# Performance work log

Measured on AMD Instinct MI355X. Metric: run time of the kernel, lower is better.

The kernel has to match this reference:

```python
import jax, jax.numpy as jnp
import numpy as np

HIDDEN = 2048
NUM_EXPERTS = 64
TOP_K = 2
LOAD_BALANCE_ALPHA = 0.01
Z_LOSS_ALPHA = 1e-4
TEMPERATURE = 1.0  # buffer init, clamped to [0.1, 2.0] -> 1.0


def setup_inputs() -> dict:
    key = jax.random.key(0)
    k1, k2 = jax.random.split(key)
    x = jax.random.normal(k1, (4, 4096, HIDDEN), dtype=jnp.float32)
    W = jax.random.normal(k2, (NUM_EXPERTS, HIDDEN), dtype=jnp.float32) * (1.0 / np.sqrt(HIDDEN))
    return {"x": x, "W": W}


def reference(x, W):
    # Eval-mode forward of RuchbahMoEGate.
    B, S, H = x.shape
    x_flat = x.reshape(-1, H)                       # [N, H], N = B*S
    logits = jnp.einsum('nh,eh->ne', x_flat, W)     # gate projection, [N, E]
    logits = logits / TEMPERATURE                   # temp clamped to [0.1,2.0]
    scores = jax.nn.softmax(logits, axis=-1)        # [N, E]
    # top-k routing (eval: dynamic top-k == top_k, no capacity limitation)
    top_scores, top_idx = jax.lax.top_k(scores, TOP_K)   # [N, K]
    top_scores = jax.nn.softmax(top_scores.astype(jnp.float32), axis=-1).astype(x.dtype)
    # load-balance loss (eval: total_routing_count == 0 -> basic term only)
    expert_load = scores.mean(axis=0)               # [E]
    ideal_load = 1.0 / NUM_EXPERTS
    lb_loss = LOAD_BALANCE_ALPHA * jnp.sum((expert_load - ideal_load) ** 2)
    # z-loss: penalize large logit logsumexp
    z_loss = Z_LOSS_ALPHA * jnp.mean(jax.nn.logsumexp(logits, axis=-1) ** 2)
    total_loss = lb_loss + z_loss
    return top_scores, top_idx, total_loss
```

## Files before the change

### kernel.cpp

```cpp
#include <hip/hip_runtime.h>
#include <cstdint>
#include <cstddef>

#define HDIM 2048
#define NEXP 64
#define HC   16
#define BTOK 128
#define GTHR 128
#define PX   132
#define PW   68
#define GATE_TOK 16

__global__ __launch_bounds__(GTHR) void moe_gemm(const float* __restrict__ x,
                                                 const float* __restrict__ W,
                                                 float* __restrict__ partial,
                                                 int N, int HS) {
  __shared__ __align__(16) float xt[2][HC][PX];
  __shared__ __align__(16) float wt[2][HC][PW];

  const int ntb   = N / BTOK;
  const int tb    = blockIdx.x % ntb;
  const int hsIdx = blockIdx.x / ntb;
  const int tok0  = tb * BTOK;
  const int h0    = hsIdx * HS;
  const int tid   = threadIdx.x;
  const int lane  = tid & 63;
  const int wid   = tid >> 6;
  const int xoff  = wid * 64 + (lane >> 3) * 8;
  const int e0    = (lane & 7) * 8;
  const int srow  = tid >> 2;
  const int sj    = (tid & 3) * 4;

  float acc[8][8];
#pragma unroll
  for (int t = 0; t < 8; ++t)
#pragma unroll
    for (int e = 0; e < 8; ++e) acc[t][e] = 0.f;

  float4 xr[4], wr[2];

#pragma unroll
  for (int i = 0; i < 4; ++i)
    xr[i] = *reinterpret_cast<const float4*>(&x[(size_t)(tok0 + srow + i * 32) * HDIM + h0 + sj]);
#pragma unroll
  for (int i = 0; i < 2; ++i)
    wr[i] = *reinterpret_cast<const float4*>(&W[(size_t)(srow + i * 32) * HDIM + h0 + sj]);
#pragma unroll
  for (int i = 0; i < 4; ++i) {
    const int r = srow + i * 32;
    xt[0][sj + 0][r] = xr[i].x; xt[0][sj + 1][r] = xr[i].y;
    xt[0][sj + 2][r] = xr[i].z; xt[0][sj + 3][r] = xr[i].w;
  }
#pragma unroll
  for (int i = 0; i < 2; ++i) {
    const int r = srow + i * 32;
    wt[0][sj + 0][r] = wr[i].x; wt[0][sj + 1][r] = wr[i].y;
    wt[0][sj + 2][r] = wr[i].z; wt[0][sj + 3][r] = wr[i].w;
  }
  __syncthreads();

  const int niter = HS / HC;
  int cur = 0;
  for (int c = 0; c < niter; ++c) {
    if (c + 1 < niter) {
      const int hb = h0 + (c + 1) * HC;
#pragma unroll
      for (int i = 0; i < 4; ++i)
        xr[i] = *reinterpret_cast<const float4*>(&x[(size_t)(tok0 + srow + i * 32) * HDIM + hb + sj]);
#pragma unroll
      for (int i = 0; i < 2; ++i)
        wr[i] = *reinterpret_cast<const float4*>(&W[(size_t)(srow + i * 32) * HDIM + hb + sj]);
    }
#pragma unroll
    for (int h = 0; h < HC; ++h) {
      const float4 a0 = *reinterpret_cast<const float4*>(&xt[cur][h][xoff]);
      const float4 a1 = *reinterpret_cast<const float4*>(&xt[cur][h][xoff + 4]);
      const float4 b0 = *reinterpret_cast<const float4*>(&wt[cur][h][e0]);
      const float4 b1 = *reinterpret_cast<const float4*>(&wt[cur][h][e0 + 4]);
      const float xs[8] = {a0.x, a0.y, a0.z, a0.w, a1.x, a1.y, a1.z, a1.w};
      const float wv[8] = {b0.x, b0.y, b0.z, b0.w, b1.x, b1.y, b1.z, b1.w};
#pragma unroll
      for (int t = 0; t < 8; ++t)
#pragma unroll
        for (int e = 0; e < 8; ++e)
          acc[t][e] = fmaf(xs[t], wv[e], acc[t][e]);
    }
    if (c + 1 < niter) {
      const int nx = cur ^ 1;
#pragma unroll
      for (int i = 0; i < 4; ++i) {
        const int r = srow + i * 32;
        xt[nx][sj + 0][r] = xr[i].x; xt[nx][sj + 1][r] = xr[i].y;
        xt[nx][sj + 2][r] = xr[i].z; xt[nx][sj + 3][r] = xr[i].w;
      }
#pragma unroll
      for (int i = 0; i < 2; ++i) {
        const int r = srow + i * 32;
        wt[nx][sj + 0][r] = wr[i].x; wt[nx][sj + 1][r] = wr[i].y;
        wt[nx][sj + 2][r] = wr[i].z; wt[nx][sj + 3][r] = wr[i].w;
      }
    }
    __syncthreads();
    cur ^= 1;
  }

  const size_t base = ((size_t)hsIdx * N + (tok0 + xoff)) * NEXP + e0;
#pragma unroll
  for (int t = 0; t < 8; ++t) {
    *reinterpret_cast<float4*>(&partial[base + (size_t)t * NEXP]) =
        make_float4(acc[t][0], acc[t][1], acc[t][2], acc[t][3]);
    *reinterpret_cast<float4*>(&partial[base + (size_t)t * NEXP + 4]) =
        make_float4(acc[t][4], acc[t][5], acc[t][6], acc[t][7]);
  }
}

template <int HSPLIT>
__global__ __launch_bounds__(256) void moe_gate(const float* __restrict__ partial,
                                                int N,
                                                float* __restrict__ outS,
                                                float* __restrict__ outI,
                                                float* __restrict__ esumP,
                                                float* __restrict__ lse2P) {
  __shared__ float es[4][NEXP];
  __shared__ float l2[4];
  const int tid  = threadIdx.x;
  const int lane = tid & 63;
  const int w    = tid >> 6;
  const int base = blockIdx.x * GATE_TOK + w * 4;

  float esum = 0.f, lse2 = 0.f;
#pragma unroll
  for (int tt = 0; tt < 4; ++tt) {
    const int t = base + tt;
    float logit = 0.f;
#pragma unroll
    for (int hs = 0; hs < HSPLIT; ++hs)
      logit += partial[((size_t)hs * N + t) * NEXP + lane];

    float m = logit;
#pragma unroll
    for (int d = 1; d < 64; d <<= 1) m = fmaxf(m, __shfl_xor(m, d));
    const float p = expf(logit - m);
    float s = p;
#pragma unroll
    for (int d = 1; d < 64; d <<= 1) s += __shfl_xor(s, d);
    const float score = p / s;

    float v1 = score; int i1 = lane;
#pragma unroll
    for (int d = 1; d < 64; d <<= 1) {
      const float pv = __shfl_xor(v1, d);
      const int   pi = __shfl_xor(i1, d);
      if (pv > v1 || (pv == v1 && pi < i1)) { v1 = pv; i1 = pi; }
    }
    float v2 = (lane == i1) ? -1.f : score; int i2 = lane;
#pragma unroll
    for (int d = 1; d < 64; d <<= 1) {
      const float pv = __shfl_xor(v2, d);
      const int   pi = __shfl_xor(i2, d);
      if (pv > v2 || (pv == v2 && pi < i2)) { v2 = pv; i2 = pi; }
    }

    if (lane == 0) {
      const float mx  = fmaxf(v1, v2);
      const float e1  = expf(v1 - mx), e2 = expf(v2 - mx);
      const float inv = 1.f / (e1 + e2);
      *reinterpret_cast<float2*>(&outS[2 * (size_t)t]) = make_float2(e1 * inv, e2 * inv);
      *reinterpret_cast<float2*>(&outI[2 * (size_t)t]) = make_float2((float)i1, (float)i2);
    }

    esum += score;
    const float lse = m + logf(s);
    lse2 += lse * lse;
  }

  es[w][lane] = esum;
  if (lane == 0) l2[w] = lse2;
  __syncthreads();
  if (tid < NEXP)
    esumP[(size_t)blockIdx.x * NEXP + tid] = es[0][tid] + es[1][tid] + es[2][tid] + es[3][tid];
  if (tid == 0)
    lse2P[blockIdx.x] = l2[0] + l2[1] + l2[2] + l2[3];
}

__global__ __launch_bounds__(256) void moe_loss(const float* __restrict__ esumP,
                                                const float* __restrict__ lse2P,
                                                float* __restrict__ outL,
                                                int N, int nb) {
  __shared__ float es[4][NEXP];
  __shared__ float l2s[4];
  const int tid = threadIdx.x, lane = tid & 63, w = tid >> 6;

  float acc = 0.f;
  for (int b = w; b < nb; b += 4) acc += esumP[(size_t)b * NEXP + lane];
  es[w][lane] = acc;

  float la = 0.f;
  for (int b = tid; b < nb; b += 256) la += lse2P[b];
#pragma unroll
  for (int d = 1; d < 64; d <<= 1) la += __shfl_xor(la, d);
  if (lane == 0) l2s[w] = la;
  __syncthreads();

  if (tid < NEXP) {
    const float tot  = es[0][tid] + es[1][tid] + es[2][tid] + es[3][tid];
    const float load = tot / (float)N;
    const float dv   = load - 1.0f / 64.0f;
    float q = dv * dv;
#pragma unroll
    for (int d = 1; d < 64; d <<= 1) q += __shfl_xor(q, d);
    if (tid == 0) {
      const float lseSum = l2s[0] + l2s[1] + l2s[2] + l2s[3];
      outL[0] = 0.01f * q + 1e-4f * (lseSum / (float)N);
    }
  }
}

extern "C" void kernel_launch(void* const* d_in, const int* in_sizes, int n_in,
                              void* d_out, int out_size, void* d_ws, size_t ws_size,
                              hipStream_t stream) {
  const float* x = (const float*)d_in[0];
  const float* W = (const float*)d_in[1];
  const int N  = in_sizes[0] / HDIM;
  const int GB = N / GATE_TOK;

  float* out  = (float*)d_out;
  float* outS = out;
  float* outI = out + (size_t)2 * N;
  float* outL = out + (size_t)4 * N;

  int hsplit = 1;
  for (int h = 8; h >= 1; h >>= 1) {
    const size_t need = (size_t)h * N * NEXP * sizeof(float)
                      + (size_t)GB * (NEXP + 1) * sizeof(float) + 256;
    if (ws_size >= need) { hsplit = h; break; }
  }
  const int HS = HDIM / hsplit;

  float* partial = (float*)d_ws;
  float* esumP   = (float*)((char*)d_ws + (size_t)hsplit * N * NEXP * sizeof(float));
  float* lse2P   = esumP + (size_t)GB * NEXP;

  const int ntb = N / BTOK;
  moe_gemm<<<dim3(ntb * hsplit), dim3(GTHR), 0, stream>>>(x, W, partial, N, HS);
  switch (hsplit) {
    case 8: moe_gate<8><<<dim3(GB), dim3(256), 0, stream>>>(partial, N, outS, outI, esumP, lse2P); break;
    case 4: moe_gate<4><<<dim3(GB), dim3(256), 0, stream>>>(partial, N, outS, outI, esumP, lse2P); break;
    case 2: moe_gate<2><<<dim3(GB), dim3(256), 0, stream>>>(partial, N, outS, outI, esumP, lse2P); break;
    default: moe_gate<1><<<dim3(GB), dim3(256), 0, stream>>>(partial, N, outS, outI, esumP, lse2P); break;
  }
  moe_loss<<<dim3(1), dim3(256), 0, stream>>>(esumP, lse2P, outL, N, GB);
}
```

Measured before the change: 300.7 us.

## Shrink GEMM token tile, batch gate reductions, fuse loss via last-block atomic

The GEMM block shrinks to one 64-thread wavefront covering 64 tokens, which doubles the grid and so raises parallelism across CUs, at the cost of less reuse of W per block. The gate kernel now loads all split partials up front and interleaves the shuffle reductions for four tokens to expose ILP. The separate loss kernel is removed: the last gate block, found with an atomic counter, does the final reduction over a transposed esum buffer. This saves one launch but adds a memset and a fence/atomic per block.

```diff
diff --git a/kernel.cpp b/kernel.cpp
--- a/kernel.cpp
+++ b/kernel.cpp
@@ -5,16 +5,15 @@
 #define HDIM 2048
 #define NEXP 64
 #define HC   16
-#define BTOK 128
-#define GTHR 128
-#define PX   132
+#define BTOK 64
+#define PX   68
 #define PW   68
 #define GATE_TOK 16
 
-__global__ __launch_bounds__(GTHR) void moe_gemm(const float* __restrict__ x,
-                                                 const float* __restrict__ W,
-                                                 float* __restrict__ partial,
-                                                 int N, int HS) {
+__global__ __launch_bounds__(64) void moe_gemm(const float* __restrict__ x,
+                                               const float* __restrict__ W,
+                                               float* __restrict__ partial,
+                                               int N, int HS) {
   __shared__ __align__(16) float xt[2][HC][PX];
   __shared__ __align__(16) float wt[2][HC][PW];
 
@@ -24,10 +23,8 @@
   const int tok0  = tb * BTOK;
   const int h0    = hsIdx * HS;
   const int tid   = threadIdx.x;
-  const int lane  = tid & 63;
-  const int wid   = tid >> 6;
-  const int xoff  = wid * 64 + (lane >> 3) * 8;
-  const int e0    = (lane & 7) * 8;
+  const int xoff  = (tid >> 3) * 8;
+  const int e0    = (tid & 7) * 8;
   const int srow  = tid >> 2;
   const int sj    = (tid & 3) * 4;
 
@@ -37,23 +34,18 @@
 #pragma unroll
     for (int e = 0; e < 8; ++e) acc[t][e] = 0.f;
 
-  float4 xr[4], wr[2];
-
-#pragma unroll
-  for (int i = 0; i < 4; ++i)
-    xr[i] = *reinterpret_cast<const float4*>(&x[(size_t)(tok0 + srow + i * 32) * HDIM + h0 + sj]);
-#pragma unroll
-  for (int i = 0; i < 2; ++i)
-    wr[i] = *reinterpret_cast<const float4*>(&W[(size_t)(srow + i * 32) * HDIM + h0 + sj]);
+  float4 xr[4], wr[4];
+
 #pragma unroll
   for (int i = 0; i < 4; ++i) {
-    const int r = srow + i * 32;
+    xr[i] = *reinterpret_cast<const float4*>(&x[(size_t)(tok0 + srow + i * 16) * HDIM + h0 + sj]);
+    wr[i] = *reinterpret_cast<const float4*>(&W[(size_t)(srow + i * 16) * HDIM + h0 + sj]);
+  }
+#pragma unroll
+  for (int i = 0; i < 4; ++i) {
+    const int r = srow + i * 16;
     xt[0][sj + 0][r] = xr[i].x; xt[0][sj + 1][r] = xr[i].y;
     xt[0][sj + 2][r] = xr[i].z; xt[0][sj + 3][r] = xr[i].w;
-  }
-#pragma unroll
-  for (int i = 0; i < 2; ++i) {
-    const int r = srow + i * 32;
     wt[0][sj + 0][r] = wr[i].x; wt[0][sj + 1][r] = wr[i].y;
     wt[0][sj + 2][r] = wr[i].z; wt[0][sj + 3][r] = wr[i].w;
   }
@@ -65,11 +57,10 @@
     if (c + 1 < niter) {
       const int hb = h0 + (c + 1) * HC;
 #pragma unroll
-      for (int i = 0; i < 4; ++i)
-        xr[i] = *reinterpret_cast<const float4*>(&x[(size_t)(tok0 + srow + i * 32) * HDIM + hb + sj]);
-#pragma unroll
-      for (int i = 0; i < 2; ++i)
-        wr[i] = *reinterpret_cast<const float4*>(&W[(size_t)(srow + i * 32) * HDIM + hb + sj]);
+      for (int i = 0; i < 4; ++i) {
+        xr[i] = *reinterpret_cast<const float4*>(&x[(size_t)(tok0 + srow + i * 16) * HDIM + hb + sj]);
+        wr[i] = *reinterpret_cast<const float4*>(&W[(size_t)(srow + i * 16) * HDIM + hb + sj]);
+      }
     }
 #pragma unroll
     for (int h = 0; h < HC; ++h) {
@@ -89,13 +80,9 @@
       const int nx = cur ^ 1;
 #pragma unroll
       for (int i = 0; i < 4; ++i) {
-        const int r = srow + i * 32;
+        const int r = srow + i * 16;
         xt[nx][sj + 0][r] = xr[i].x; xt[nx][sj + 1][r] = xr[i].y;
         xt[nx][sj + 2][r] = xr[i].z; xt[nx][sj + 3][r] = xr[i].w;
-      }
-#pragma unroll
-      for (int i = 0; i < 2; ++i) {
-        const int r = srow + i * 32;
         wt[nx][sj + 0][r] = wr[i].x; wt[nx][sj + 1][r] = wr[i].y;
         wt[nx][sj + 2][r] = wr[i].z; wt[nx][sj + 3][r] = wr[i].w;
       }
@@ -116,102 +103,142 @@
 
 template <int HSPLIT>
 __global__ __launch_bounds__(256) void moe_gate(const float* __restrict__ partial,
-                                                int N,
+                                                int N, int GB,
                                                 float* __restrict__ outS,
                                                 float* __restrict__ outI,
                                                 float* __restrict__ esumP,
-                                                float* __restrict__ lse2P) {
+                                                float* __restrict__ lse2P,
+                                                unsigned* __restrict__ counter,
+                                                float* __restrict__ outL) {
   __shared__ float es[4][NEXP];
   __shared__ float l2[4];
+  __shared__ float esF[NEXP];
+  __shared__ float l2F[4];
+  __shared__ int lastFlag;
   const int tid  = threadIdx.x;
   const int lane = tid & 63;
   const int w    = tid >> 6;
   const int base = blockIdx.x * GATE_TOK + w * 4;
 
-  float esum = 0.f, lse2 = 0.f;
+  float v[4][HSPLIT];
+#pragma unroll
+  for (int tt = 0; tt < 4; ++tt)
+#pragma unroll
+    for (int hs = 0; hs < HSPLIT; ++hs)
+      v[tt][hs] = partial[((size_t)hs * N + base + tt) * NEXP + lane];
+
+  float logit[4];
 #pragma unroll
   for (int tt = 0; tt < 4; ++tt) {
-    const int t = base + tt;
-    float logit = 0.f;
-#pragma unroll
-    for (int hs = 0; hs < HSPLIT; ++hs)
-      logit += partial[((size_t)hs * N + t) * NEXP + lane];
-
-    float m = logit;
-#pragma unroll
-    for (int d = 1; d < 64; d <<= 1) m = fmaxf(m, __shfl_xor(m, d));
-    const float p = expf(logit - m);
-    float s = p;
-#pragma unroll
-    for (int d = 1; d < 64; d <<= 1) s += __shfl_xor(s, d);
-    const float score = p / s;
-
-    float v1 = score; int i1 = lane;
-#pragma unroll
-    for (int d = 1; d < 64; d <<= 1) {
-      const float pv = __shfl_xor(v1, d);
-      const int   pi = __shfl_xor(i1, d);
-      if (pv > v1 || (pv == v1 && pi < i1)) { v1 = pv; i1 = pi; }
-    }
-    float v2 = (lane == i1) ? -1.f : score; int i2 = lane;
-#pragma unroll
-    for (int d = 1; d < 64; d <<= 1) {
-      const float pv = __shfl_xor(v2, d);
-      const int   pi = __shfl_xor(i2, d);
-      if (pv > v2 || (pv == v2 && pi < i2)) { v2 = pv; i2 = pi; }
-    }
-
-    if (lane == 0) {
-      const float mx  = fmaxf(v1, v2);
-      const float e1  = expf(v1 - mx), e2 = expf(v2 - mx);
+    float s = v[tt][0];
+#pragma unroll
+    for (int hs = 1; hs < HSPLIT; ++hs) s += v[tt][hs];
+    logit[tt] = s;
+  }
+
+  float m[4], p[4], s[4], sc[4];
+#pragma unroll
+  for (int tt = 0; tt < 4; ++tt) m[tt] = logit[tt];
+#pragma unroll
+  for (int d = 1; d < 64; d <<= 1)
+#pragma unroll
+    for (int tt = 0; tt < 4; ++tt) m[tt] = fmaxf(m[tt], __shfl_xor(m[tt], d));
+#pragma unroll
+  for (int tt = 0; tt < 4; ++tt) { p[tt] = expf(logit[tt] - m[tt]); s[tt] = p[tt]; }
+#pragma unroll
+  for (int d = 1; d < 64; d <<= 1)
+#pragma unroll
+    for (int tt = 0; tt < 4; ++tt) s[tt] += __shfl_xor(s[tt], d);
+#pragma unroll
+  for (int tt = 0; tt < 4; ++tt) sc[tt] = p[tt] / s[tt];
+
+  float v1[4]; int i1[4];
+#pragma unroll
+  for (int tt = 0; tt < 4; ++tt) { v1[tt] = sc[tt]; i1[tt] = lane; }
+#pragma unroll
+  for (int d = 1; d < 64; d <<= 1)
+#pragma unroll
+    for (int tt = 0; tt < 4; ++tt) {
+      const float pv = __shfl_xor(v1[tt], d);
+      const int   pi = __shfl_xor(i1[tt], d);
+      if (pv > v1[tt] || (pv == v1[tt] && pi < i1[tt])) { v1[tt] = pv; i1[tt] = pi; }
+    }
+  float v2[4]; int i2[4];
+#pragma unroll
+  for (int tt = 0; tt < 4; ++tt) { v2[tt] = (lane == i1[tt]) ? -1.f : sc[tt]; i2[tt] = lane; }
+#pragma unroll
+  for (int d = 1; d < 64; d <<= 1)
+#pragma unroll
+    for (int tt = 0; tt < 4; ++tt) {
+      const float pv = __shfl_xor(v2[tt], d);
+      const int   pi = __shfl_xor(i2[tt], d);
+      if (pv > v2[tt] || (pv == v2[tt] && pi < i2[tt])) { v2[tt] = pv; i2[tt] = pi; }
+    }
+
+  if (lane == 0) {
+#pragma unroll
+    for (int tt = 0; tt < 4; ++tt) {
+      const int t = base + tt;
+      const float mx  = fmaxf(v1[tt], v2[tt]);
+      const float e1  = expf(v1[tt] - mx), e2 = expf(v2[tt] - mx);
       const float inv = 1.f / (e1 + e2);
       *reinterpret_cast<float2*>(&outS[2 * (size_t)t]) = make_float2(e1 * inv, e2 * inv);
-      *reinterpret_cast<float2*>(&outI[2 * (size_t)t]) = make_float2((float)i1, (float)i2);
-    }
-
-    esum += score;
-    const float lse = m + logf(s);
+      *reinterpret_cast<float2*>(&outI[2 * (size_t)t]) = make_float2((float)i1[tt], (float)i2[tt]);
+    }
+  }
+
+  const float esum = ((sc[0] + sc[1]) + sc[2]) + sc[3];
+  float lse2 = 0.f;
+#pragma unroll
+  for (int tt = 0; tt < 4; ++tt) {
+    const float lse = m[tt] + logf(s[tt]);
     lse2 += lse * lse;
   }
-
   es[w][lane] = esum;
   if (lane == 0) l2[w] = lse2;
   __syncthreads();
   if (tid < NEXP)
-    esumP[(size_t)blockIdx.x * NEXP + tid] = es[0][tid] + es[1][tid] + es[2][tid] + es[3][tid];
+    esumP[(size_t)tid * GB + blockIdx.x] = es[0][tid] + es[1][tid] + es[2][tid] + es[3][tid];
   if (tid == 0)
     lse2P[blockIdx.x] = l2[0] + l2[1] + l2[2] + l2[3];
-}
-
-__global__ __launch_bounds__(256) void moe_loss(const float* __restrict__ esumP,
-                                                const float* __restrict__ lse2P,
-                                                float* __restrict__ outL,
-                                                int N, int nb) {
-  __shared__ float es[4][NEXP];
-  __shared__ float l2s[4];
-  const int tid = threadIdx.x, lane = tid & 63, w = tid >> 6;
-
-  float acc = 0.f;
-  for (int b = w; b < nb; b += 4) acc += esumP[(size_t)b * NEXP + lane];
-  es[w][lane] = acc;
+
+  __threadfence();
+  if (tid == 0) lastFlag = (atomicAdd(counter, 1u) == (unsigned)(GB - 1));
+  __syncthreads();
+  if (!lastFlag) return;
+  __threadfence();
+
+  const int e = tid >> 2, q = tid & 3;
+  const int seg = GB / 4;
+  const float4* colp = reinterpret_cast<const float4*>(&esumP[(size_t)e * GB + q * seg]);
+  float a = 0.f;
+  for (int i = 0; i < seg / 4; ++i) {
+    const float4 t4 = colp[i];
+    a += ((t4.x + t4.y) + t4.z) + t4.w;
+  }
+  a += __shfl_xor(a, 1);
+  a += __shfl_xor(a, 2);
+  if (q == 0) esF[e] = a;
 
   float la = 0.f;
-  for (int b = tid; b < nb; b += 256) la += lse2P[b];
+  for (int i = tid; i * 4 < GB; i += 256) {
+    const float4 t4 = reinterpret_cast<const float4*>(lse2P)[i];
+    la += ((t4.x + t4.y) + t4.z) + t4.w;
+  }
 #pragma unroll
   for (int d = 1; d < 64; d <<= 1) la += __shfl_xor(la, d);
-  if (lane == 0) l2s[w] = la;
+  if (lane == 0) l2F[w] = la;
   __syncthreads();
 
   if (tid < NEXP) {
-    const float tot  = es[0][tid] + es[1][tid] + es[2][tid] + es[3][tid];
-    const float load = tot / (float)N;
+    const float load = esF[tid] / (float)N;
     const float dv   = load - 1.0f / 64.0f;
-    float q = dv * dv;
-#pragma unroll
-    for (int d = 1; d < 64; d <<= 1) q += __shfl_xor(q, d);
+    float qq = dv * dv;
+#pragma unroll
+    for (int d = 1; d < 64; d <<= 1) qq += __shfl_xor(qq, d);
     if (tid == 0) {
-      const float lseSum = l2s[0] + l2s[1] + l2s[2] + l2s[3];
-      outL[0] = 0.01f * q + 1e-4f * (lseSum / (float)N);
+      const float lseSum = ((l2F[0] + l2F[1]) + l2F[2]) + l2F[3];
+      outL[0] = 0.01f * qq + 1e-4f * (lseSum / (float)N);
     }
   }
 }
@@ -232,22 +259,25 @@
   int hsplit = 1;
   for (int h = 8; h >= 1; h >>= 1) {
     const size_t need = (size_t)h * N * NEXP * sizeof(float)
-                      + (size_t)GB * (NEXP + 1) * sizeof(float) + 256;
+                      + (size_t)NEXP * GB * sizeof(float)
+                      + (size_t)GB * sizeof(float) + 256;
     if (ws_size >= need) { hsplit = h; break; }
   }
   const int HS = HDIM / hsplit;
 
-  float* partial = (float*)d_ws;
-  float* esumP   = (float*)((char*)d_ws + (size_t)hsplit * N * NEXP * sizeof(float));
-  float* lse2P   = esumP + (size_t)GB * NEXP;
+  float*    partial = (float*)d_ws;
+  float*    esumP   = (float*)((char*)d_ws + (size_t)hsplit * N * NEXP * 4);
+  float*    lse2P   = esumP + (size_t)NEXP * GB;
+  unsigned* counter = (unsigned*)(lse2P + GB);
+
+  hipMemsetAsync(counter, 0, sizeof(unsigned), stream);
 
   const int ntb = N / BTOK;
-  moe_gemm<<<dim3(ntb * hsplit), dim3(GTHR), 0, stream>>>(x, W, partial, N, HS);
+  moe_gemm<<<dim3(ntb * hsplit), dim3(64), 0, stream>>>(x, W, partial, N, HS);
   switch (hsplit) {
-    case 8: moe_gate<8><<<dim3(GB), dim3(256), 0, stream>>>(partial, N, outS, outI, esumP, lse2P); break;
-    case 4: moe_gate<4><<<dim3(GB), dim3(256), 0, stream>>>(partial, N, outS, outI, esumP, lse2P); break;
-    case 2: moe_gate<2><<<dim3(GB), dim3(256), 0, stream>>>(partial, N, outS, outI, esumP, lse2P); break;
-    default: moe_gate<1><<<dim3(GB), dim3(256), 0, stream>>>(partial, N, outS, outI, esumP, lse2P); break;
-  }
-  moe_loss<<<dim3(1), dim3(256), 0, stream>>>(esumP, lse2P, outL, N, GB);
+    case 8: moe_gate<8><<<dim3(GB), dim3(256), 0, stream>>>(partial, N, GB, outS, outI, esumP, lse2P, counter, outL); break;
+    case 4: moe_gate<4><<<dim3(GB), dim3(256), 0, stream>>>(partial, N, GB, outS, outI, esumP, lse2P, counter, outL); break;
+    case 2: moe_gate<2><<<dim3(GB), dim3(256), 0, stream>>>(partial, N, GB, outS, outI, esumP, lse2P, counter, outL); break;
+    default: moe_gate<1><<<dim3(GB), dim3(256), 0, stream>>>(partial, N, GB, outS, outI, esumP, lse2P, counter, outL); break;
+  }
 }
```

New measurement: 363.3 us. 1.21x slower.
